# Performance work log

Hardware: AMD Instinct MI355X
Metric: run time of the kernel (lower is better)

The kernel has to match this reference:

```python
import jax, jax.numpy as jnp
import numpy as np

B, C_OUT, DIM_I, DIM_J, DIM_K = 4, 32, 32, 32, 32


def setup_inputs() -> dict:
    key = jax.random.key(0)
    k1, k2, k3 = jax.random.split(key, 3)
    L = DIM_I * DIM_J * DIM_K
    ys = jax.random.normal(k1, (B, 12, C_OUT, L), jnp.float32)
    # Conv3d(12*c_out, c_out, kernel_size=1) -> pointwise, weight [c_out, 12*c_out]
    conv_w = jax.random.normal(k2, (C_OUT, 12 * C_OUT), jnp.float32) / np.sqrt(12 * C_OUT).astype(np.float32)
    conv_b = jax.random.normal(k3, (C_OUT,), jnp.float32) * 0.01
    gamma = jnp.ones((C_OUT,), jnp.float32)
    beta = jnp.zeros((C_OUT,), jnp.float32)
    return {"ys": ys, "conv_w": conv_w, "conv_b": conv_b,
            "gamma": gamma, "beta": beta, "i": DIM_I, "j": DIM_J, "k": DIM_K}


def _merge(x, i, j, k):
    # x: [B, 4, C, L] with L = i*j*k; 4 scan directions
    Bd, _, C, L = x.shape
    x0, x1, x2, x3 = x[:, 0], x[:, 1], x[:, 2], x[:, 3]
    # forward scans + flipped reverse scans, concat on channel dim
    x_0_2 = jnp.concatenate([x0, x2[..., ::-1]], axis=1)  # [B, 2C, L]
    x_1_3 = jnp.concatenate([x1, x3[..., ::-1]], axis=1)  # [B, 2C, L]
    a = x_0_2.reshape(Bd, 2 * C, i, j, k)
    b = x_1_3.reshape(Bd, 2 * C, i, k, j).swapaxes(-2, -1)  # transpose(-2,-1)
    return jnp.concatenate([a, b], axis=1)  # [B, 4C, i, j, k]


def reference(ys, conv_w, conv_b, gamma, beta, i, j, k):
    # ys: [B, 12, C, i*j*k]
    xs_i = _merge(ys[:, 0:4], i, j, k)                                  # [B,4C,i,j,k]
    xs_j = jnp.transpose(_merge(ys[:, 4:8], j, k, i), (0, 1, 4, 2, 3))  # b c j k i -> b c i j k
    xs_k = jnp.transpose(_merge(ys[:, 8:12], k, i, j), (0, 1, 3, 4, 2)) # b c k i j -> b c i j k
    xs = jnp.concatenate([xs_i, xs_j, xs_k], axis=1)                    # [B,12C,i,j,k]
    # 1x1x1 Conv3d == channel GEMM
    out = jnp.einsum('bcijk,oc->boijk', xs, conv_w) + conv_b[None, :, None, None, None]
    # BatchNorm3d, training mode: batch stats over (B, i, j, k), biased var, eps=1e-5
    mean = out.mean(axis=(0, 2, 3, 4))
    var = out.var(axis=(0, 2, 3, 4))
    eps = 1e-5
    inv = jax.lax.rsqrt(var + eps)
    out = (out - mean[None, :, None, None, None]) * inv[None, :, None, None, None]
    return out * gamma[None, :, None, None, None] + beta[None, :, None, None, None]
```

## Files before the change

kernel.cpp:

```cpp
#include <hip/hip_runtime.h>
#include <stdint.h>

#define COUT 32

__device__ const int T_SRC[12] = {0,2,1,3,4,6,5,7,8,10,9,11};
__device__ const int T_SI[12]  = {1024,-1024,1024,-1024,1,-1,32,-32,32,-32,1,-1};
__device__ const int T_SJ[12]  = {32,-32,1,-1,1024,-1024,1024,-1024,1,-1,32,-32};
__device__ const int T_SK[12]  = {1,-1,32,-32,32,-32,1,-1,1024,-1024,1024,-1024};
__device__ const int T_RB[12]  = {0,32767,0,32767,0,32767,0,32767,0,32767,0,32767};
__device__ const int T_CB[12]  = {0,0,0,0,1,1,0,0,0,0,1,1};

typedef __attribute__((address_space(3))) unsigned int as3u;
typedef __attribute__((address_space(1))) unsigned int as1u;

__device__ __forceinline__ void stage_phase(
    const float* __restrict__ ys, float* lbuf, int ph,
    int b, int i0, int j0, int k0, int wv, int lhi, int llo)
{
  const int s  = T_SRC[ph];
  const int Si = T_SI[ph], Sj = T_SJ[ph], Sk = T_SK[ph];
  const int rb = T_RB[ph];
  const float* ybase = ys + (((size_t)((b*12 + s)*COUT + wv*4)) << 15);
  if (!T_CB[ph]) {
    const int sc0 = rb + i0*Si + j0*Sj + k0*Sk + lhi*Sj + llo*Sk;
#pragma unroll
    for (int cc = 0; cc < 4; ++cc) {
#pragma unroll
      for (int pr = 0; pr < 8; ++pr) {
        const float* src = ybase + (((size_t)cc) << 15) + (sc0 + pr*Si);
        float* dst = lbuf + (wv*4 + cc)*512 + pr*64;
        __builtin_amdgcn_global_load_lds((const as1u*)src, (as3u*)dst, 4, 0, 0);
      }
    }
  } else {
    const int e   = llo ^ lhi;
    const int sc0 = rb + i0*Si + j0*Sj + k0*Sk + lhi*Sk;
#pragma unroll
    for (int cc = 0; cc < 4; ++cc) {
#pragma unroll
      for (int pr = 0; pr < 8; ++pr) {
        const int diq = e ^ pr;
        const float* src = ybase + (((size_t)cc) << 15) + (sc0 + pr*Sj + diq*Si);
        float* dst = lbuf + (wv*4 + cc)*512 + pr*64;
        __builtin_amdgcn_global_load_lds((const as1u*)src, (as3u*)dst, 4, 0, 0);
      }
    }
  }
}

__device__ __forceinline__ void compute_phase(
    const float* __restrict__ w, const float* lbuf, int ph, int sidx, float* acc)
{
  const float* wp = w + ph*COUT;
#pragma unroll
  for (int c4 = 0; c4 < 8; ++c4) {
    const float x0 = lbuf[(c4*4+0)*512 + sidx];
    const float x1 = lbuf[(c4*4+1)*512 + sidx];
    const float x2 = lbuf[(c4*4+2)*512 + sidx];
    const float x3 = lbuf[(c4*4+3)*512 + sidx];
#pragma unroll
    for (int o = 0; o < COUT; ++o) {
      const float4 wq = *(const float4*)(wp + o*384 + c4*4);
      acc[o] = __builtin_fmaf(x0, wq.x, acc[o]);
      acc[o] = __builtin_fmaf(x1, wq.y, acc[o]);
      acc[o] = __builtin_fmaf(x2, wq.z, acc[o]);
      acc[o] = __builtin_fmaf(x3, wq.w, acc[o]);
    }
  }
}

__global__ __launch_bounds__(512, 2) void k_fused(
    const float* __restrict__ ys, const float* __restrict__ w,
    const float* __restrict__ cb, float* __restrict__ out)
{
  __shared__ float lds[2][COUT*512];
  const int tid  = threadIdx.x;
  const int lane = tid & 63, wv = tid >> 6;
  const int lhi  = lane >> 3, llo = lane & 7;
  const int bid  = blockIdx.x;
  const int b  = bid >> 6;
  const int i0 = ((bid >> 4) & 3) * 8;
  const int j0 = ((bid >> 2) & 3) * 8;
  const int k0 = (bid & 3) * 8;

  const int di = tid >> 6, dj = (tid >> 3) & 7, dk = tid & 7;
  const int sidxA = tid;
  const int sidxB = dj*64 + dk*8 + (di ^ dk ^ dj);

  float acc[COUT];
#pragma unroll
  for (int o = 0; o < COUT; ++o) acc[o] = 0.f;

  stage_phase(ys, &lds[0][0], 0, b, i0, j0, k0, wv, lhi, llo);
  for (int ph = 0; ph < 12; ++ph) {
    float* cur = &lds[ph & 1][0];
    if (ph < 11) {
      stage_phase(ys, &lds[(ph + 1) & 1][0], ph + 1, b, i0, j0, k0, wv, lhi, llo);
      asm volatile("s_waitcnt vmcnt(32)" ::: "memory");
    } else {
      asm volatile("s_waitcnt vmcnt(0)" ::: "memory");
    }
    __builtin_amdgcn_s_barrier();
    const int sidx = T_CB[ph] ? sidxB : sidxA;
    compute_phase(w, cur, ph, sidx, acc);
    asm volatile("" ::: "memory");
    __builtin_amdgcn_s_barrier();
  }

  const int gpos = (i0 + di)*1024 + (j0 + dj)*32 + (k0 + dk);
  float* op = out + ((((size_t)b) * COUT) << 15) + gpos;
#pragma unroll
  for (int o = 0; o < COUT; ++o)
    op[((size_t)o) << 15] = acc[o] + cb[o];
}

__global__ __launch_bounds__(256, 4) void k_stats(
    const float* __restrict__ out, float* __restrict__ stats)
{
  __shared__ float red[8];
  const int bid = blockIdx.x;
  const int o   = bid & 31;
  const int tid = threadIdx.x;
  const float* p = out + (((size_t)bid) << 15);
  float s1 = 0.f, s2 = 0.f;
#pragma unroll 4
  for (int it = 0; it < 32; ++it) {
    const float4 v = *(const float4*)(p + it*1024 + tid*4);
    s1 += (v.x + v.y) + (v.z + v.w);
    s2 += (v.x*v.x + v.y*v.y) + (v.z*v.z + v.w*v.w);
  }
#pragma unroll
  for (int off = 32; off > 0; off >>= 1) {
    s1 += __shfl_down(s1, off, 64);
    s2 += __shfl_down(s2, off, 64);
  }
  if ((tid & 63) == 0) { red[(tid >> 6)*2] = s1; red[(tid >> 6)*2 + 1] = s2; }
  __syncthreads();
  if (tid == 0) {
    atomicAdd(&stats[o],      red[0] + red[2] + red[4] + red[6]);
    atomicAdd(&stats[32 + o], red[1] + red[3] + red[5] + red[7]);
  }
}

__global__ __launch_bounds__(256, 4) void k_norm(
    float* __restrict__ out, const float* __restrict__ stats,
    const float* __restrict__ gamma, const float* __restrict__ beta)
{
  const int bid = blockIdx.x;
  const int o   = bid & 31;
  const int tid = threadIdx.x;
  const float invN = 1.0f / 131072.0f;
  const float mean = stats[o] * invN;
  const float var  = stats[32 + o] * invN - mean*mean;
  const float inv  = rsqrtf(var + 1e-5f);
  const float sc   = gamma[o] * inv;
  const float sh   = beta[o] - mean * sc;
  float* p = out + (((size_t)bid) << 15);
#pragma unroll 4
  for (int it = 0; it < 32; ++it) {
    float4 v = *(const float4*)(p + it*1024 + tid*4);
    v.x = __builtin_fmaf(v.x, sc, sh);
    v.y = __builtin_fmaf(v.y, sc, sh);
    v.z = __builtin_fmaf(v.z, sc, sh);
    v.w = __builtin_fmaf(v.w, sc, sh);
    *(float4*)(p + it*1024 + tid*4) = v;
  }
}

extern "C" void kernel_launch(void* const* d_in, const int* in_sizes, int n_in,
                              void* d_out, int out_size, void* d_ws, size_t ws_size,
                              hipStream_t stream)
{
  const float* ys    = (const float*)d_in[0];
  const float* w     = (const float*)d_in[1];
  const float* cb    = (const float*)d_in[2];
  const float* gamma = (const float*)d_in[3];
  const float* beta  = (const float*)d_in[4];
  float* out   = (float*)d_out;
  float* stats = (float*)d_ws;

  hipMemsetAsync(stats, 0, 64 * sizeof(float), stream);
  hipLaunchKernelGGL(k_fused, dim3(256), dim3(512), 0, stream, ys, w, cb, out);
  hipLaunchKernelGGL(k_stats, dim3(128), dim3(256), 0, stream, out, stats);
  hipLaunchKernelGGL(k_norm,  dim3(128), dim3(256), 0, stream, out, stats, gamma, beta);
}
```

Baseline: 479.4 us.

## Stage per-phase weights in LDS and widen stats/norm grids

Each phase's 32x32 weight slice is now prefetched into a double-buffered LDS area with async global-to-LDS loads from wave 0, replacing per-thread global float4 weight reads inside the FMA loop. Constant phase tables in device memory are replaced by computed parameters, removing those scalar global loads. The stats and normalization kernels are split into four blocks per channel row (512 blocks), raising parallelism across CUs. The changes add wait-count bookkeeping that differs between waves, and more atomic adds in the stats kernel.

```diff
diff --git a/kernel.cpp b/kernel.cpp
--- a/kernel.cpp
+++ b/kernel.cpp
@@ -3,25 +3,36 @@
 
 #define COUT 32
 
-__device__ const int T_SRC[12] = {0,2,1,3,4,6,5,7,8,10,9,11};
-__device__ const int T_SI[12]  = {1024,-1024,1024,-1024,1,-1,32,-32,32,-32,1,-1};
-__device__ const int T_SJ[12]  = {32,-32,1,-1,1024,-1024,1024,-1024,1,-1,32,-32};
-__device__ const int T_SK[12]  = {1,-1,32,-32,32,-32,1,-1,1024,-1024,1024,-1024};
-__device__ const int T_RB[12]  = {0,32767,0,32767,0,32767,0,32767,0,32767,0,32767};
-__device__ const int T_CB[12]  = {0,0,0,0,1,1,0,0,0,0,1,1};
-
 typedef __attribute__((address_space(3))) unsigned int as3u;
 typedef __attribute__((address_space(1))) unsigned int as1u;
+
+__device__ __forceinline__ void phase_params(int ph, int& src, int& Si, int& Sj, int& Sk,
+                                             int& rb, int& cb) {
+  const int g = ph >> 2, q = ph & 3;
+  const int neg = q & 1, v = q >> 1;
+  src = (ph & ~3) | (neg << 1) | v;
+  rb = neg ? 32767 : 0;
+  const int sA = v ? 1 : 32, sB = v ? 32 : 1;
+  if (g == 0)      { Si = 1024; Sj = sA; Sk = sB; }
+  else if (g == 1) { Sj = 1024; Sk = sA; Si = sB; }
+  else             { Sk = 1024; Si = sA; Sj = sB; }
+  if (neg) { Si = -Si; Sj = -Sj; Sk = -Sk; }
+  cb = ((g == 1) && (v == 0)) || ((g == 2) && (v == 1));
+}
+
+__device__ __forceinline__ int phase_cb(int ph) {
+  const int g = ph >> 2, v = (ph >> 1) & 1;
+  return ((g == 1) && (v == 0)) || ((g == 2) && (v == 1));
+}
 
 __device__ __forceinline__ void stage_phase(
     const float* __restrict__ ys, float* lbuf, int ph,
     int b, int i0, int j0, int k0, int wv, int lhi, int llo)
 {
-  const int s  = T_SRC[ph];
-  const int Si = T_SI[ph], Sj = T_SJ[ph], Sk = T_SK[ph];
-  const int rb = T_RB[ph];
+  int s, Si, Sj, Sk, rb, cb;
+  phase_params(ph, s, Si, Sj, Sk, rb, cb);
   const float* ybase = ys + (((size_t)((b*12 + s)*COUT + wv*4)) << 15);
-  if (!T_CB[ph]) {
+  if (!cb) {
     const int sc0 = rb + i0*Si + j0*Sj + k0*Sk + lhi*Sj + llo*Sk;
 #pragma unroll
     for (int cc = 0; cc < 4; ++cc) {
@@ -48,10 +59,19 @@
   }
 }
 
+__device__ __forceinline__ void stage_weights(const float* __restrict__ w, float* wbuf,
+                                              int ph, int lane) {
+  const float* src0 = w + ph*32 + (lane >> 3)*384 + (lane & 7)*4;
+#pragma unroll
+  for (int qq = 0; qq < 4; ++qq) {
+    __builtin_amdgcn_global_load_lds((const as1u*)(src0 + qq*8*384),
+                                     (as3u*)(wbuf + qq*256), 16, 0, 0);
+  }
+}
+
 __device__ __forceinline__ void compute_phase(
-    const float* __restrict__ w, const float* lbuf, int ph, int sidx, float* acc)
-{
-  const float* wp = w + ph*COUT;
+    const float* wbuf, const float* lbuf, int sidx, float* acc)
+{
 #pragma unroll
   for (int c4 = 0; c4 < 8; ++c4) {
     const float x0 = lbuf[(c4*4+0)*512 + sidx];
@@ -60,7 +80,7 @@
     const float x3 = lbuf[(c4*4+3)*512 + sidx];
 #pragma unroll
     for (int o = 0; o < COUT; ++o) {
-      const float4 wq = *(const float4*)(wp + o*384 + c4*4);
+      const float4 wq = *(const float4*)(wbuf + o*32 + c4*4);
       acc[o] = __builtin_fmaf(x0, wq.x, acc[o]);
       acc[o] = __builtin_fmaf(x1, wq.y, acc[o]);
       acc[o] = __builtin_fmaf(x2, wq.z, acc[o]);
@@ -74,6 +94,7 @@
     const float* __restrict__ cb, float* __restrict__ out)
 {
   __shared__ float lds[2][COUT*512];
+  __shared__ float wlds[2][COUT*32];
   const int tid  = threadIdx.x;
   const int lane = tid & 63, wv = tid >> 6;
   const int lhi  = lane >> 3, llo = lane & 7;
@@ -92,17 +113,24 @@
   for (int o = 0; o < COUT; ++o) acc[o] = 0.f;
 
   stage_phase(ys, &lds[0][0], 0, b, i0, j0, k0, wv, lhi, llo);
+  if (wv == 0) stage_weights(w, &wlds[0][0], 0, lane);
   for (int ph = 0; ph < 12; ++ph) {
-    float* cur = &lds[ph & 1][0];
+    const float* cur  = &lds[ph & 1][0];
+    const float* wcur = &wlds[ph & 1][0];
     if (ph < 11) {
       stage_phase(ys, &lds[(ph + 1) & 1][0], ph + 1, b, i0, j0, k0, wv, lhi, llo);
-      asm volatile("s_waitcnt vmcnt(32)" ::: "memory");
+      if (wv == 0) {
+        stage_weights(w, &wlds[(ph + 1) & 1][0], ph + 1, lane);
+        asm volatile("s_waitcnt vmcnt(36)" ::: "memory");
+      } else {
+        asm volatile("s_waitcnt vmcnt(32)" ::: "memory");
+      }
     } else {
       asm volatile("s_waitcnt vmcnt(0)" ::: "memory");
     }
     __builtin_amdgcn_s_barrier();
-    const int sidx = T_CB[ph] ? sidxB : sidxA;
-    compute_phase(w, cur, ph, sidx, acc);
+    const int sidx = phase_cb(ph) ? sidxB : sidxA;
+    compute_phase(wcur, cur, sidx, acc);
     asm volatile("" ::: "memory");
     __builtin_amdgcn_s_barrier();
   }
@@ -118,13 +146,13 @@
     const float* __restrict__ out, float* __restrict__ stats)
 {
   __shared__ float red[8];
-  const int bid = blockIdx.x;
-  const int o   = bid & 31;
+  const int row = blockIdx.x >> 2, quad = blockIdx.x & 3;
+  const int o   = row & 31;
   const int tid = threadIdx.x;
-  const float* p = out + (((size_t)bid) << 15);
+  const float* p = out + (((size_t)row) << 15) + quad * 8192;
   float s1 = 0.f, s2 = 0.f;
-#pragma unroll 4
-  for (int it = 0; it < 32; ++it) {
+#pragma unroll
+  for (int it = 0; it < 8; ++it) {
     const float4 v = *(const float4*)(p + it*1024 + tid*4);
     s1 += (v.x + v.y) + (v.z + v.w);
     s2 += (v.x*v.x + v.y*v.y) + (v.z*v.z + v.w*v.w);
@@ -146,8 +174,8 @@
     float* __restrict__ out, const float* __restrict__ stats,
     const float* __restrict__ gamma, const float* __restrict__ beta)
 {
-  const int bid = blockIdx.x;
-  const int o   = bid & 31;
+  const int row = blockIdx.x >> 2, quad = blockIdx.x & 3;
+  const int o   = row & 31;
   const int tid = threadIdx.x;
   const float invN = 1.0f / 131072.0f;
   const float mean = stats[o] * invN;
@@ -155,9 +183,9 @@
   const float inv  = rsqrtf(var + 1e-5f);
   const float sc   = gamma[o] * inv;
   const float sh   = beta[o] - mean * sc;
-  float* p = out + (((size_t)bid) << 15);
-#pragma unroll 4
-  for (int it = 0; it < 32; ++it) {
+  float* p = out + (((size_t)row) << 15) + quad * 8192;
+#pragma unroll
+  for (int it = 0; it < 8; ++it) {
     float4 v = *(const float4*)(p + it*1024 + tid*4);
     v.x = __builtin_fmaf(v.x, sc, sh);
     v.y = __builtin_fmaf(v.y, sc, sh);
@@ -181,6 +209,6 @@
 
   hipMemsetAsync(stats, 0, 64 * sizeof(float), stream);
   hipLaunchKernelGGL(k_fused, dim3(256), dim3(512), 0, stream, ys, w, cb, out);
-  hipLaunchKernelGGL(k_stats, dim3(128), dim3(256), 0, stream, out, stats);
-  hipLaunchKernelGGL(k_norm,  dim3(128), dim3(256), 0, stream, out, stats, gamma, beta);
-}
+  hipLaunchKernelGGL(k_stats, dim3(512), dim3(256), 0, stream, out, stats);
+  hipLaunchKernelGGL(k_norm,  dim3(512), dim3(256), 0, stream, out, stats, gamma, beta);
+}
```

Result: faster. 424.5 us (-11.5%).
